# Kernel tuning notes

Measured on AMD Instinct MI355X. Metric: run time of the kernel, lower is better.

Reference implementation:

```python
import jax, jax.numpy as jnp
import numpy as np

B, C, H, W = 8, 512, 32, 32
N_HEADS = 4
D_K = C // N_HEADS  # 128


def setup_inputs() -> dict:
    key = jax.random.key(0)
    k1, k2, k3, k4, k5 = jax.random.split(key, 5)
    x = jax.random.normal(k1, (B, C, H, W), dtype=jnp.float32)
    # projection: Linear(in_ch, n_heads*d_k*3)
    Wp = jax.random.normal(k2, (C, N_HEADS * D_K * 3), dtype=jnp.float32) * (C ** -0.5)
    bp = jax.random.normal(k3, (N_HEADS * D_K * 3,), dtype=jnp.float32) * 0.01
    # output: Linear(n_heads*d_k, in_ch)
    Wo = jax.random.normal(k4, (N_HEADS * D_K, C), dtype=jnp.float32) * ((N_HEADS * D_K) ** -0.5)
    bo = jax.random.normal(k5, (C,), dtype=jnp.float32) * 0.01
    return {"x": x, "Wp": Wp, "bp": bp, "Wo": Wo, "bo": bo}


def reference(x, Wp, bp, Wo, bo):
    b, c, h, w = x.shape
    scale = D_K ** -0.5
    # [B, C, H, W] -> [B, N, C], N = H*W
    xs = x.reshape(b, c, h * w).transpose(0, 2, 1)
    qkv = (xs @ Wp + bp).reshape(b, h * w, N_HEADS, 3 * D_K)
    q, k, v = jnp.split(qkv, 3, axis=-1)  # each [B, N, H, D]
    attn = jnp.einsum('bihd,bjhd->bijh', q, k) * scale
    attn = jax.nn.softmax(attn, axis=2)  # softmax over j (keys)
    out = jnp.einsum('bijh,bjhd->bihd', attn, v)
    out = out.reshape(b, h * w, N_HEADS * D_K)
    out = out @ Wo + bo
    out = out + xs  # residual (note: GroupNorm is unused in the original forward)
    return out.transpose(0, 2, 1).reshape(b, c, h, w)
```

## Files before the change

kernel.cpp:

```cpp
#include <hip/hip_runtime.h>

#define NB 8
#define NC 512
#define NTOK 1024
#define NHEADS 4
#define DKH 128

typedef unsigned short u16;
typedef __attribute__((ext_vector_type(8))) short bf16x8;
typedef __attribute__((ext_vector_type(4))) float f32x4;

__device__ inline u16 f2b(float f) {
    union { float f; unsigned u; } v; v.f = f;
    unsigned r = v.u + 0x7fffu + ((v.u >> 16) & 1u);
    return (u16)(r >> 16);
}

__device__ __forceinline__ void gll16(const u16* g, u16* l) {
    __builtin_amdgcn_global_load_lds((const __attribute__((address_space(1))) unsigned*)g,
                                     (__attribute__((address_space(3))) unsigned*)l, 16, 0, 0);
}

__global__ __launch_bounds__(256) void t_f32_bf16(const float* __restrict__ in, u16* __restrict__ out,
                                                  int R, int Cc, long inBatch, long outBatch)
{
    __shared__ float tile[32][33];
    const float* src = in + (long)blockIdx.z * inBatch;
    u16* dst = out + (long)blockIdx.z * outBatch;
    int c0 = blockIdx.x * 32, r0 = blockIdx.y * 32;
    int tx = threadIdx.x, ty = threadIdx.y;
    #pragma unroll
    for (int k = 0; k < 4; ++k)
        tile[ty + 8*k][tx] = src[(long)(r0 + ty + 8*k) * Cc + c0 + tx];
    __syncthreads();
    #pragma unroll
    for (int k = 0; k < 4; ++k)
        dst[(long)(c0 + ty + 8*k) * R + r0 + tx] = f2b(tile[tx][ty + 8*k]);
}

__global__ __launch_bounds__(256) void gemm_qkv(const u16* __restrict__ WpT, const u16* __restrict__ xsb,
                                                const float* __restrict__ bp,
                                                u16* __restrict__ qg, u16* __restrict__ kg, u16* __restrict__ vg)
{
    __shared__ union SmU {
        struct { u16 As[128][72]; u16 Bs[128][72]; } s;
        u16 Os[4][64][72];
    } sm;
    const int tid = threadIdx.x;
    const int m0 = blockIdx.x * 128;
    const int n0 = blockIdx.y * 128;
    const int w = tid >> 6, lane = tid & 63, quad = lane >> 4, lc = lane & 15;
    const int mo = (w & 1) * 64, no = (w >> 1) * 64;

    f32x4 acc[4][4] = {};

    for (int k0 = 0; k0 < NC; k0 += 64) {
        #pragma unroll
        for (int p = 0; p < 4; ++p) {
            int id = p * 256 + tid;
            int row = id >> 3, cp = (id & 7) << 3;
            *(bf16x8*)&sm.s.As[row][cp] = *(const bf16x8*)&WpT[(long)(m0 + row) * NC + k0 + cp];
            *(bf16x8*)&sm.s.Bs[row][cp] = *(const bf16x8*)&xsb[(long)(n0 + row) * NC + k0 + cp];
        }
        __syncthreads();
        #pragma unroll
        for (int ks = 0; ks < 2; ++ks) {
            bf16x8 af[4], bfr[4];
            #pragma unroll
            for (int t = 0; t < 4; ++t) {
                af[t]  = *(const bf16x8*)&sm.s.As[mo + t*16 + lc][ks*32 + quad*8];
                bfr[t] = *(const bf16x8*)&sm.s.Bs[no + t*16 + lc][ks*32 + quad*8];
            }
            #pragma unroll
            for (int mt = 0; mt < 4; ++mt)
                #pragma unroll
                for (int nt = 0; nt < 4; ++nt)
                    acc[mt][nt] = __builtin_amdgcn_mfma_f32_16x16x32_bf16(af[mt], bfr[nt], acc[mt][nt], 0, 0, 0);
        }
        __syncthreads();
    }

    const int bb = n0 >> 10;
    const int nblk = n0 & 1023;
    const int cqb = m0 + mo;
    const int h = cqb / 384;
    const int rem = cqb - h * 384;
    const int sel = rem >> 7;
    const int d_base = rem & 127;

    #pragma unroll
    for (int mt = 0; mt < 4; ++mt) {
        int cq0 = cqb + mt*16 + quad*4;
        float b0 = bp[cq0+0], b1 = bp[cq0+1], b2 = bp[cq0+2], b3 = bp[cq0+3];
        #pragma unroll
        for (int nt = 0; nt < 4; ++nt) {
            f32x4 a = acc[mt][nt];
            int nl = nt*16 + lc;
            int ml = mt*16 + quad*4;
            u16 e0 = f2b(a[0]+b0), e1 = f2b(a[1]+b1), e2 = f2b(a[2]+b2), e3 = f2b(a[3]+b3);
            if (sel == 2) {
                sm.Os[w][ml+0][nl] = e0; sm.Os[w][ml+1][nl] = e1;
                sm.Os[w][ml+2][nl] = e2; sm.Os[w][ml+3][nl] = e3;
            } else {
                sm.Os[w][nl][ml+0] = e0; sm.Os[w][nl][ml+1] = e1;
                sm.Os[w][nl][ml+2] = e2; sm.Os[w][nl][ml+3] = e3;
            }
        }
    }
    __builtin_amdgcn_sched_barrier(0);

    const long bhbase = (long)(bb * NHEADS + h);
    const int sw = (((lane & 7) ^ (lane >> 3)) << 3);
    if (sel == 2) {
        #pragma unroll
        for (int pass = 0; pass < 8; ++pass) {
            int ml  = pass*8 + (lane >> 3);
            int nl0 = (lane & 7) * 8;
            bf16x8 vv = *(const bf16x8*)&sm.Os[w][ml][nl0];
            *(bf16x8*)&vg[((bhbase*DKH + d_base + ml) << 10) + nblk + no + sw] = vv;
        }
    } else if (sel == 1) {
        #pragma unroll
        for (int pass = 0; pass < 8; ++pass) {
            int nl  = pass*8 + (lane >> 3);
            int ml0 = (lane & 7) * 8;
            bf16x8 vv = *(const bf16x8*)&sm.Os[w][nl][ml0];
            *(bf16x8*)&kg[((bhbase*NTOK + nblk + no + nl) << 7) + d_base + sw] = vv;
        }
    } else {
        #pragma unroll
        for (int pass = 0; pass < 8; ++pass) {
            int nl  = pass*8 + (lane >> 3);
            int ml0 = (lane & 7) * 8;
            bf16x8 vv = *(const bf16x8*)&sm.Os[w][nl][ml0];
            *(bf16x8*)&qg[((bhbase*NTOK + nblk + no + nl) << 7) + d_base + ml0] = vv;
        }
    }
}

__global__ __launch_bounds__(256) void attn(const u16* __restrict__ qg, const u16* __restrict__ kg,
                                            const u16* __restrict__ vtg, u16* __restrict__ ho)
{
    __shared__ u16 Ks[2][64*128];
    __shared__ u16 Vt[2][128*64];
    __shared__ u16 Ps[4][16][72];
    const int tid = threadIdx.x;
    const int w = tid >> 6, lane = tid & 63, quad = lane >> 4, lc = lane & 15;
    const int h = blockIdx.y, b = blockIdx.z;
    const int i0 = blockIdx.x * 64 + w * 16;
    const long bh = (long)(b * NHEADS + h) << 17;
    const u16* qb = qg + bh;
    const u16* kb = kg + bh;
    const u16* vb = vtg + bh;
    const float SL2E = 0.08838834764831845f * 1.4426950408889634f;

    bf16x8 qf[4];
    #pragma unroll
    for (int ks = 0; ks < 4; ++ks)
        qf[ks] = *(const bf16x8*)&qb[(long)(i0 + lc) * DKH + ks*32 + quad*8];

    f32x4 o[8] = {};
    float lsum = 0.f;
    const int xs = lc & 7;

    #pragma unroll
    for (int p = 0; p < 4; ++p) {
        int ck = (w*4+p)*64 + lane;
        gll16(&kb[(long)ck * 8], &Ks[0][(w*4+p)*512]);
        gll16(&vb[(((long)(ck >> 3)) << 10) + (ck & 7)*8], &Vt[0][(w*4+p)*512]);
    }

    for (int t = 0; t < 16; ++t) {
        __syncthreads();
        if (t < 15) {
            long jo = (long)(t+1) * 64;
            #pragma unroll
            for (int p = 0; p < 4; ++p) {
                int ck = (w*4+p)*64 + lane;
                gll16(&kb[jo*128 + (long)ck*8], &Ks[(t+1)&1][(w*4+p)*512]);
                gll16(&vb[(((long)(ck >> 3)) << 10) + jo + (ck & 7)*8], &Vt[(t+1)&1][(w*4+p)*512]);
            }
        }
        const u16* K = Ks[t&1];
        const u16* V = Vt[t&1];

        f32x4 s[4] = {};
        #pragma unroll
        for (int ks = 0; ks < 4; ++ks)
            #pragma unroll
            for (int jt = 0; jt < 4; ++jt) {
                bf16x8 kf = *(const bf16x8*)&K[(jt*16 + lc)*128 + (((ks*4 + quad) ^ xs) << 3)];
                s[jt] = __builtin_amdgcn_mfma_f32_16x16x32_bf16(kf, qf[ks], s[jt], 0, 0, 0);
            }

        #pragma unroll
        for (int jt = 0; jt < 4; ++jt) {
            float p0 = __builtin_amdgcn_exp2f(s[jt][0] * SL2E);
            float p1 = __builtin_amdgcn_exp2f(s[jt][1] * SL2E);
            float p2 = __builtin_amdgcn_exp2f(s[jt][2] * SL2E);
            float p3 = __builtin_amdgcn_exp2f(s[jt][3] * SL2E);
            lsum += (p0 + p1) + (p2 + p3);
            ushort4 pk;
            pk.x = f2b(p0); pk.y = f2b(p1); pk.z = f2b(p2); pk.w = f2b(p3);
            *(ushort4*)&Ps[w][lc][jt*16 + quad*4] = pk;
        }
        __builtin_amdgcn_sched_barrier(0);

        #pragma unroll
        for (int ks2 = 0; ks2 < 2; ++ks2) {
            bf16x8 pf = *(const bf16x8*)&Ps[w][lc][ks2*32 + quad*8];
            #pragma unroll
            for (int dt = 0; dt < 8; ++dt) {
                bf16x8 vf = *(const bf16x8*)&V[(dt*16 + lc)*64 + (((ks2*4 + quad) ^ xs) << 3)];
                o[dt] = __builtin_amdgcn_mfma_f32_16x16x32_bf16(vf, pf, o[dt], 0, 0, 0);
            }
        }
    }

    lsum += __shfl_xor(lsum, 16);
    lsum += __shfl_xor(lsum, 32);
    float inv = 1.0f / lsum;

    #pragma unroll
    for (int dt = 0; dt < 8; ++dt) {
        ushort4 pk;
        pk.x = f2b(o[dt][0] * inv); pk.y = f2b(o[dt][1] * inv);
        pk.z = f2b(o[dt][2] * inv); pk.w = f2b(o[dt][3] * inv);
        *(ushort4*)&ho[(long)(b*NTOK + i0 + lc) * NC + h*DKH + dt*16 + quad*4] = pk;
    }
}

__global__ __launch_bounds__(256) void gemm_out(const u16* __restrict__ WoT, const u16* __restrict__ ho,
                                                const float* __restrict__ bo, const float* __restrict__ xin,
                                                float* __restrict__ dout)
{
    __shared__ u16 As[128][72];
    __shared__ u16 Bs[128][72];
    const int tid = threadIdx.x;
    const int m0 = blockIdx.x * 128;
    const int n0 = blockIdx.y * 128;
    const int w = tid >> 6, lane = tid & 63, quad = lane >> 4, lc = lane & 15;
    const int mo = (w & 1) * 64, no = (w >> 1) * 64;

    f32x4 acc[4][4] = {};

    for (int k0 = 0; k0 < NC; k0 += 64) {
        #pragma unroll
        for (int p = 0; p < 4; ++p) {
            int id = p * 256 + tid;
            int row = id >> 3, cp = (id & 7) << 3;
            *(bf16x8*)&As[row][cp] = *(const bf16x8*)&WoT[(long)(m0 + row) * NC + k0 + cp];
            *(bf16x8*)&Bs[row][cp] = *(const bf16x8*)&ho[(long)(n0 + row) * NC + k0 + cp];
        }
        __syncthreads();
        #pragma unroll
        for (int ks = 0; ks < 2; ++ks) {
            bf16x8 af[4], bfr[4];
            #pragma unroll
            for (int t = 0; t < 4; ++t) {
                af[t]  = *(const bf16x8*)&As[mo + t*16 + lc][ks*32 + quad*8];
                bfr[t] = *(const bf16x8*)&Bs[no + t*16 + lc][ks*32 + quad*8];
            }
            #pragma unroll
            for (int mt = 0; mt < 4; ++mt)
                #pragma unroll
                for (int nt = 0; nt < 4; ++nt)
                    acc[mt][nt] = __builtin_amdgcn_mfma_f32_16x16x32_bf16(af[mt], bfr[nt], acc[mt][nt], 0, 0, 0);
        }
        __syncthreads();
    }

    const int bb = n0 >> 10;
    #pragma unroll
    for (int mt = 0; mt < 4; ++mt) {
        int cc0 = m0 + mo + mt*16 + quad*4;
        float b0 = bo[cc0+0], b1 = bo[cc0+1], b2 = bo[cc0+2], b3 = bo[cc0+3];
        #pragma unroll
        for (int nt = 0; nt < 4; ++nt) {
            int nl = (n0 + no + nt*16 + lc) & (NTOK - 1);
            f32x4 a = acc[mt][nt];
            long ix = ((long)(bb*NC + cc0) << 10) + nl;
            dout[ix]             = a[0] + b0 + xin[ix];
            dout[ix + (1 << 10)] = a[1] + b1 + xin[ix + (1 << 10)];
            dout[ix + (2 << 10)] = a[2] + b2 + xin[ix + (2 << 10)];
            dout[ix + (3 << 10)] = a[3] + b3 + xin[ix + (3 << 10)];
        }
    }
}

extern "C" void kernel_launch(void* const* d_in, const int* in_sizes, int n_in,
                              void* d_out, int out_size, void* d_ws, size_t ws_size,
                              hipStream_t stream)
{
    (void)in_sizes; (void)n_in; (void)out_size; (void)ws_size;
    const float* x  = (const float*)d_in[0];
    const float* Wp = (const float*)d_in[1];
    const float* bp = (const float*)d_in[2];
    const float* Wo = (const float*)d_in[3];
    const float* bo = (const float*)d_in[4];
    float* out = (float*)d_out;

    u16* ws  = (u16*)d_ws;
    u16* xsb = ws;
    u16* WpT = xsb + (long)NB * NTOK * NC;
    u16* WoT = WpT + 1536L * 512;
    u16* qg  = WoT + 512L * 512;
    u16* kg  = qg + (long)NB * NHEADS * NTOK * DKH;
    u16* vtg = kg + (long)NB * NHEADS * NTOK * DKH;
    u16* ho  = vtg + (long)NB * NHEADS * NTOK * DKH;

    dim3 tb(32, 8);
    t_f32_bf16<<<dim3(NTOK/32, NC/32, NB), tb, 0, stream>>>(x, xsb, NC, NTOK, (long)NC*NTOK, (long)NTOK*NC);
    t_f32_bf16<<<dim3(1536/32, 512/32, 1), tb, 0, stream>>>(Wp, WpT, 512, 1536, 0, 0);
    t_f32_bf16<<<dim3(512/32, 512/32, 1), tb, 0, stream>>>(Wo, WoT, 512, 512, 0, 0);

    gemm_qkv<<<dim3(1536/128, (NB*NTOK)/128), 256, 0, stream>>>(WpT, xsb, bp, qg, kg, vtg);
    attn<<<dim3(NTOK/64, NHEADS, NB), 256, 0, stream>>>(qg, kg, vtg, ho);
    gemm_out<<<dim3(NC/128, (NB*NTOK)/128), 256, 0, stream>>>(WoT, ho, bo, x, out);
}
```

Before: 156.9 us.

## Merge prep transposes, use direct-to-LDS swizzled loads, retile attention and output GEMM

The three transpose/convert launches are merged into one prep launch that picks its source by blockIdx.z. Both GEMMs now stage tiles with global_load_lds into XOR-swizzled, unpadded LDS in place of register round-trips. The attention kernel moves to 512-thread blocks covering 128 queries on a 1D grid ordered by XCD, so each K/V tile load is shared by twice as many query rows. The output GEMM uses 128x64 tiles to launch more blocks. These changes target launch overhead, LDS staging cost, K/V reuse and occupancy, at the cost of fewer resident waves for the larger attention blocks.

```diff
diff --git a/kernel.cpp b/kernel.cpp
--- a/kernel.cpp
+++ b/kernel.cpp
@@ -21,12 +21,17 @@
                                      (__attribute__((address_space(3))) unsigned*)l, 16, 0, 0);
 }
 
-__global__ __launch_bounds__(256) void t_f32_bf16(const float* __restrict__ in, u16* __restrict__ out,
-                                                  int R, int Cc, long inBatch, long outBatch)
+__global__ __launch_bounds__(256) void prep(const float* __restrict__ x, const float* __restrict__ Wp,
+                                            const float* __restrict__ Wo,
+                                            u16* __restrict__ xsb, u16* __restrict__ WpT, u16* __restrict__ WoT)
 {
     __shared__ float tile[32][33];
-    const float* src = in + (long)blockIdx.z * inBatch;
-    u16* dst = out + (long)blockIdx.z * outBatch;
+    const int z = blockIdx.z;
+    const float* src; u16* dst; int R, Cc;
+    if (z == 0)      { src = Wp; dst = WpT; R = 512; Cc = 1536; }
+    else if (z == 1) { if (blockIdx.x >= 16) return; src = Wo; dst = WoT; R = 512; Cc = 512; }
+    else             { if (blockIdx.x >= 32) return;
+                       src = x + (long)(z-2)*NC*NTOK; dst = xsb + (long)(z-2)*NTOK*NC; R = NC; Cc = NTOK; }
     int c0 = blockIdx.x * 32, r0 = blockIdx.y * 32;
     int tx = threadIdx.x, ty = threadIdx.y;
     #pragma unroll
@@ -43,7 +48,7 @@
                                                 u16* __restrict__ qg, u16* __restrict__ kg, u16* __restrict__ vg)
 {
     __shared__ union SmU {
-        struct { u16 As[128][72]; u16 Bs[128][72]; } s;
+        struct { u16 As[128][64]; u16 Bs[128][64]; } s;
         u16 Os[4][64][72];
     } sm;
     const int tid = threadIdx.x;
@@ -51,16 +56,18 @@
     const int n0 = blockIdx.y * 128;
     const int w = tid >> 6, lane = tid & 63, quad = lane >> 4, lc = lane & 15;
     const int mo = (w & 1) * 64, no = (w >> 1) * 64;
+    const int sw8 = (((lane & 7) ^ (lane >> 3)) << 3);
+    const int xs = lc & 7;
 
     f32x4 acc[4][4] = {};
 
     for (int k0 = 0; k0 < NC; k0 += 64) {
+        __syncthreads();
         #pragma unroll
         for (int p = 0; p < 4; ++p) {
-            int id = p * 256 + tid;
-            int row = id >> 3, cp = (id & 7) << 3;
-            *(bf16x8*)&sm.s.As[row][cp] = *(const bf16x8*)&WpT[(long)(m0 + row) * NC + k0 + cp];
-            *(bf16x8*)&sm.s.Bs[row][cp] = *(const bf16x8*)&xsb[(long)(n0 + row) * NC + k0 + cp];
+            int row = w*32 + p*8 + (lane >> 3);
+            gll16(&WpT[(long)(m0 + row) * NC + k0 + sw8], &sm.s.As[w*32 + p*8][0]);
+            gll16(&xsb[(long)(n0 + row) * NC + k0 + sw8], &sm.s.Bs[w*32 + p*8][0]);
         }
         __syncthreads();
         #pragma unroll
@@ -68,8 +75,8 @@
             bf16x8 af[4], bfr[4];
             #pragma unroll
             for (int t = 0; t < 4; ++t) {
-                af[t]  = *(const bf16x8*)&sm.s.As[mo + t*16 + lc][ks*32 + quad*8];
-                bfr[t] = *(const bf16x8*)&sm.s.Bs[no + t*16 + lc][ks*32 + quad*8];
+                af[t]  = *(const bf16x8*)&sm.s.As[mo + t*16 + lc][((ks*4 + quad) ^ xs) << 3];
+                bfr[t] = *(const bf16x8*)&sm.s.Bs[no + t*16 + lc][((ks*4 + quad) ^ xs) << 3];
             }
             #pragma unroll
             for (int mt = 0; mt < 4; ++mt)
@@ -77,8 +84,8 @@
                 for (int nt = 0; nt < 4; ++nt)
                     acc[mt][nt] = __builtin_amdgcn_mfma_f32_16x16x32_bf16(af[mt], bfr[nt], acc[mt][nt], 0, 0, 0);
         }
-        __syncthreads();
-    }
+    }
+    __syncthreads();
 
     const int bb = n0 >> 10;
     const int nblk = n0 & 1023;
@@ -110,7 +117,7 @@
     __builtin_amdgcn_sched_barrier(0);
 
     const long bhbase = (long)(bb * NHEADS + h);
-    const int sw = (((lane & 7) ^ (lane >> 3)) << 3);
+    const int sw = sw8;
     if (sel == 2) {
         #pragma unroll
         for (int pass = 0; pass < 8; ++pass) {
@@ -138,16 +145,19 @@
     }
 }
 
-__global__ __launch_bounds__(256) void attn(const u16* __restrict__ qg, const u16* __restrict__ kg,
+__global__ __launch_bounds__(512) void attn(const u16* __restrict__ qg, const u16* __restrict__ kg,
                                             const u16* __restrict__ vtg, u16* __restrict__ ho)
 {
     __shared__ u16 Ks[2][64*128];
     __shared__ u16 Vt[2][128*64];
-    __shared__ u16 Ps[4][16][72];
+    __shared__ u16 Ps[8][16][72];
     const int tid = threadIdx.x;
     const int w = tid >> 6, lane = tid & 63, quad = lane >> 4, lc = lane & 15;
-    const int h = blockIdx.y, b = blockIdx.z;
-    const int i0 = blockIdx.x * 64 + w * 16;
+    const int id = blockIdx.x;
+    const int xcd = id & 7, rest = id >> 3, sub = rest & 3, bx = rest >> 2;
+    const int pr = xcd + sub*8;
+    const int b = pr >> 2, h = pr & 3;
+    const int i0 = bx*128 + w*16;
     const long bh = (long)(b * NHEADS + h) << 17;
     const u16* qb = qg + bh;
     const u16* kb = kg + bh;
@@ -164,10 +174,10 @@
     const int xs = lc & 7;
 
     #pragma unroll
-    for (int p = 0; p < 4; ++p) {
-        int ck = (w*4+p)*64 + lane;
-        gll16(&kb[(long)ck * 8], &Ks[0][(w*4+p)*512]);
-        gll16(&vb[(((long)(ck >> 3)) << 10) + (ck & 7)*8], &Vt[0][(w*4+p)*512]);
+    for (int p = 0; p < 2; ++p) {
+        int ck = (w*2 + p)*64 + lane;
+        gll16(&kb[(long)ck * 8], &Ks[0][(w*2 + p)*512]);
+        gll16(&vb[(((long)(ck >> 3)) << 10) + (ck & 7)*8], &Vt[0][(w*2 + p)*512]);
     }
 
     for (int t = 0; t < 16; ++t) {
@@ -175,10 +185,10 @@
         if (t < 15) {
             long jo = (long)(t+1) * 64;
             #pragma unroll
-            for (int p = 0; p < 4; ++p) {
-                int ck = (w*4+p)*64 + lane;
-                gll16(&kb[jo*128 + (long)ck*8], &Ks[(t+1)&1][(w*4+p)*512]);
-                gll16(&vb[(((long)(ck >> 3)) << 10) + jo + (ck & 7)*8], &Vt[(t+1)&1][(w*4+p)*512]);
+            for (int p = 0; p < 2; ++p) {
+                int ck = (w*2 + p)*64 + lane;
+                gll16(&kb[jo*128 + (long)ck*8], &Ks[(t+1)&1][(w*2 + p)*512]);
+                gll16(&vb[(((long)(ck >> 3)) << 10) + jo + (ck & 7)*8], &Vt[(t+1)&1][(w*2 + p)*512]);
             }
         }
         const u16* K = Ks[t&1];
@@ -234,40 +244,45 @@
                                                 const float* __restrict__ bo, const float* __restrict__ xin,
                                                 float* __restrict__ dout)
 {
-    __shared__ u16 As[128][72];
-    __shared__ u16 Bs[128][72];
+    __shared__ struct { u16 As[128][64]; u16 Bs[64][64]; } sm;
     const int tid = threadIdx.x;
     const int m0 = blockIdx.x * 128;
-    const int n0 = blockIdx.y * 128;
+    const int n0 = blockIdx.y * 64;
     const int w = tid >> 6, lane = tid & 63, quad = lane >> 4, lc = lane & 15;
-    const int mo = (w & 1) * 64, no = (w >> 1) * 64;
-
-    f32x4 acc[4][4] = {};
+    const int mo = (w & 1) * 64, no = (w >> 1) * 32;
+    const int sw8 = (((lane & 7) ^ (lane >> 3)) << 3);
+    const int xs = lc & 7;
+
+    f32x4 acc[4][2] = {};
 
     for (int k0 = 0; k0 < NC; k0 += 64) {
+        __syncthreads();
         #pragma unroll
         for (int p = 0; p < 4; ++p) {
-            int id = p * 256 + tid;
-            int row = id >> 3, cp = (id & 7) << 3;
-            *(bf16x8*)&As[row][cp] = *(const bf16x8*)&WoT[(long)(m0 + row) * NC + k0 + cp];
-            *(bf16x8*)&Bs[row][cp] = *(const bf16x8*)&ho[(long)(n0 + row) * NC + k0 + cp];
+            int row = w*32 + p*8 + (lane >> 3);
+            gll16(&WoT[(long)(m0 + row) * NC + k0 + sw8], &sm.As[w*32 + p*8][0]);
+        }
+        #pragma unroll
+        for (int p = 0; p < 2; ++p) {
+            int row = w*16 + p*8 + (lane >> 3);
+            gll16(&ho[(long)(n0 + row) * NC + k0 + sw8], &sm.Bs[w*16 + p*8][0]);
         }
         __syncthreads();
         #pragma unroll
         for (int ks = 0; ks < 2; ++ks) {
-            bf16x8 af[4], bfr[4];
-            #pragma unroll
-            for (int t = 0; t < 4; ++t) {
-                af[t]  = *(const bf16x8*)&As[mo + t*16 + lc][ks*32 + quad*8];
-                bfr[t] = *(const bf16x8*)&Bs[no + t*16 + lc][ks*32 + quad*8];
-            }
+            bf16x8 af[4], bfr[2];
+            #pragma unroll
+            for (int t = 0; t < 4; ++t)
+                af[t] = *(const bf16x8*)&sm.As[mo + t*16 + lc][((ks*4 + quad) ^ xs) << 3];
+            #pragma unroll
+            for (int t = 0; t < 2; ++t)
+                bfr[t] = *(const bf16x8*)&sm.Bs[no + t*16 + lc][((ks*4 + quad) ^ xs) << 3];
             #pragma unroll
             for (int mt = 0; mt < 4; ++mt)
                 #pragma unroll
-                for (int nt = 0; nt < 4; ++nt)
+                for (int nt = 0; nt < 2; ++nt)
                     acc[mt][nt] = __builtin_amdgcn_mfma_f32_16x16x32_bf16(af[mt], bfr[nt], acc[mt][nt], 0, 0, 0);
         }
-        __syncthreads();
     }
 
     const int bb = n0 >> 10;
@@ -276,7 +291,7 @@
         int cc0 = m0 + mo + mt*16 + quad*4;
         float b0 = bo[cc0+0], b1 = bo[cc0+1], b2 = bo[cc0+2], b3 = bo[cc0+3];
         #pragma unroll
-        for (int nt = 0; nt < 4; ++nt) {
+        for (int nt = 0; nt < 2; ++nt) {
             int nl = (n0 + no + nt*16 + lc) & (NTOK - 1);
             f32x4 a = acc[mt][nt];
             long ix = ((long)(bb*NC + cc0) << 10) + nl;
@@ -309,12 +324,8 @@
     u16* vtg = kg + (long)NB * NHEADS * NTOK * DKH;
     u16* ho  = vtg + (long)NB * NHEADS * NTOK * DKH;
 
-    dim3 tb(32, 8);
-    t_f32_bf16<<<dim3(NTOK/32, NC/32, NB), tb, 0, stream>>>(x, xsb, NC, NTOK, (long)NC*NTOK, (long)NTOK*NC);
-    t_f32_bf16<<<dim3(1536/32, 512/32, 1), tb, 0, stream>>>(Wp, WpT, 512, 1536, 0, 0);
-    t_f32_bf16<<<dim3(512/32, 512/32, 1), tb, 0, stream>>>(Wo, WoT, 512, 512, 0, 0);
-
+    prep<<<dim3(48, 16, 10), dim3(32, 8), 0, stream>>>(x, Wp, Wo, xsb, WpT, WoT);
     gemm_qkv<<<dim3(1536/128, (NB*NTOK)/128), 256, 0, stream>>>(WpT, xsb, bp, qg, kg, vtg);
-    attn<<<dim3(NTOK/64, NHEADS, NB), 256, 0, stream>>>(qg, kg, vtg, ho);
-    gemm_out<<<dim3(NC/128, (NB*NTOK)/128), 256, 0, stream>>>(WoT, ho, bo, x, out);
-}
+    attn<<<dim3(256), 512, 0, stream>>>(qg, kg, vtg, ho);
+    gemm_out<<<dim3(NC/128, (NB*NTOK)/64), 256, 0, stream>>>(WoT, ho, bo, x, out);
+}
```

After: 140.7 us. 10.3% less time.
